# Kernel tuning notes

Measured on AMD Instinct MI355X. Metric: run time of the kernel, lower is better.

## Reference

```python
import jax, jax.numpy as jnp
import numpy as np

B, N = 8, 2048
DIN, DH, DE = 32, 64, 64
R = 3          # number_relations
L = 3          # num_layers -> 1 first + 1 block + 1 last
PRED_IN = DH * (L - 1) + DE  # concat: 64*2 + 64 = 192
EPS_BN = 1e-5
EPS_NORM = 1e-12


def setup_inputs() -> dict:
    key = jax.random.key(0)
    ks = jax.random.split(key, 12)
    x = jax.random.normal(ks[0], (B, N, DIN), jnp.float32)
    # relation labels in {0..R}; 0 = no edge, 1..R = relation type
    relation = jax.random.randint(ks[1], (B, N, N), 0, R + 1).astype(jnp.int32)
    # adjacency is the 0/1 edge indicator (float), as the torch code treats it
    adj = (relation > 0).astype(jnp.float32)
    s = 0.05
    w_first = jax.random.normal(ks[2], (R, DIN, DH), jnp.float32) * s
    b_first = jnp.zeros((DH,), jnp.float32)
    w_block = jax.random.normal(ks[3], (R, DH, DH), jnp.float32) * s
    b_block = jnp.zeros((DH,), jnp.float32)
    w_last = jax.random.normal(ks[4], (R, DH, DE), jnp.float32) * s
    b_last = jnp.zeros((DE,), jnp.float32)
    w_map = jax.random.normal(ks[5], (PRED_IN, DE), jnp.float32) * s
    b_map = jnp.zeros((DE,), jnp.float32)
    return {"x": x, "relation": relation, "adj": adj,
            "w_first": w_first, "b_first": b_first,
            "w_block": w_block, "b_block": b_block,
            "w_last": w_last, "b_last": b_last,
            "w_map": w_map, "b_map": b_map}


def _graph_conv(x, rel, W, b):
    # rel: [B,N,N] (int labels or float adjacency); W: [R, din, dout]
    y = jnp.zeros((x.shape[0], x.shape[1], W.shape[2]), x.dtype)
    for i in range(R):  # fixed, small relation count
        mask = (rel == (i + 1)).astype(x.dtype)            # [B,N,N]
        h = jnp.einsum('bij,bjd->bid', mask, x)            # masked aggregation
        y = y + jnp.einsum('bid,de->bie', h, W[i])
    y = y + b
    # F.normalize(p=2, dim=2): v / max(||v||, eps)
    nrm = jnp.sqrt(jnp.sum(y * y, axis=2, keepdims=True))
    return y / jnp.maximum(nrm, EPS_NORM)


def _apply_bn(x):
    # fresh BatchNorm1d(N) in training mode, affine weight=1/bias=0:
    # normalize over (batch, feature) per node index, biased variance
    mean = jnp.mean(x, axis=(0, 2), keepdims=True)
    var = jnp.mean(jnp.square(x - mean), axis=(0, 2), keepdims=True)
    return (x - mean) * jax.lax.rsqrt(var + EPS_BN)


def reference(x, relation, adj, w_first, b_first, w_block, b_block,
              w_last, b_last, w_map, b_map):
    # conv_first uses `relation`
    h = _apply_bn(jax.nn.relu(_graph_conv(x, relation, w_first, b_first)))
    out_all = [jnp.max(h, axis=1)]
    # conv_block and conv_last are (faithfully) called with `adj` as relation
    h = _apply_bn(jax.nn.relu(_graph_conv(h, adj, w_block, b_block)))
    out_all.append(jnp.max(h, axis=1))
    h = _graph_conv(h, adj, w_last, b_last)
    out_all.append(jnp.max(h, axis=1))
    output = jnp.concatenate(out_all, axis=1)        # [B, PRED_IN]
    ypred = output @ w_map + b_map                   # map_model Linear
    return (output, ypred)
```

## Files before the change

### kernel.cpp

```cpp
#include <hip/hip_runtime.h>


#define NN 2048
#define PLANE_W 1048576L

typedef short short8 __attribute__((ext_vector_type(8)));
typedef float floatx4 __attribute__((ext_vector_type(4)));

__device__ __forceinline__ unsigned short f2bf(float x) {
  unsigned u = __float_as_uint(x);
  u += 0x7FFFu + ((u >> 16) & 1u);
  return (unsigned short)(u >> 16);
}

__device__ void dev_xw_first(char* smemc, int u, int tid,
                             const float* __restrict__ x,
                             const float* __restrict__ w,
                             unsigned short* __restrict__ xws) {
  float* xs = (float*)smemc;
  float* wsh = (float*)(smemc + 64 * 33 * 4);
  const int jc = u & 31, b = (u >> 5) & 7, r = u >> 8;
  const int j0 = jc * 64;
  for (int idx = tid; idx < 64 * 32; idx += 256) {
    int row = idx >> 5, f = idx & 31;
    xs[row * 33 + f] = x[((long)b * NN + j0 + row) * 32 + f];
    wsh[idx] = w[r * 2048 + idx];
  }
  __syncthreads();
  const int j = tid & 63, g = tid >> 6;
  const int k = j0 + j;
  const int kblk = k >> 5, kq = (k >> 3) & 3, kj = k & 7;
  unsigned short* dst =
      xws + (((long)(r * 8 + b) * 64 + kblk) * 4 + g) * 512 + kj;
  float xr[32];
#pragma unroll
  for (int f = 0; f < 32; ++f) xr[f] = xs[j * 33 + f];
#pragma unroll
  for (int ii = 0; ii < 16; ++ii) {
    float acc = 0.f;
#pragma unroll
    for (int f = 0; f < 32; ++f) acc += xr[f] * wsh[f * 64 + g * 16 + ii];
    dst[(kq * 16 + ii) * 8] = f2bf(acc);
  }
  __syncthreads();
}

__global__ __launch_bounds__(256) void k_pack_xw1(const int* __restrict__ rel,
                                                  unsigned* __restrict__ planes,
                                                  const float* __restrict__ x,
                                                  const float* __restrict__ w,
                                                  unsigned short* __restrict__ xws) {
  __shared__ __align__(16) char smem[16640];
  const int bid = blockIdx.x, tid = threadIdx.x;
  if (bid < 768) dev_xw_first(smem, bid, tid, x, w, xws);
  for (long t = (long)bid * 256 + tid; t < 1048576L; t += 4096L * 256) {
    int w32 = (int)(t & 63);
    long bi = t >> 6;
    const int4* rp = (const int4*)(rel + bi * NN + w32 * 32);
    unsigned m0 = 0, m1 = 0, m2 = 0;
#pragma unroll
    for (int c = 0; c < 8; ++c) {
      int4 v = rp[c];
      int vv[4] = {v.x, v.y, v.z, v.w};
#pragma unroll
      for (int j = 0; j < 4; ++j) {
        unsigned b1 = 1u << (c * 4 + j);
        m0 |= (vv[j] == 1) ? b1 : 0u;
        m1 |= (vv[j] == 2) ? b1 : 0u;
        m2 |= (vv[j] == 3) ? b1 : 0u;
      }
    }
    long o = bi * 64 + w32;
    planes[o] = m0;
    planes[PLANE_W + o] = m1;
    planes[2 * PLANE_W + o] = m2;
  }
}

template <int NREL, bool RELU, bool POOL3>
__global__ __launch_bounds__(512) void k_gemm8(
    const unsigned* __restrict__ planes, const unsigned short* __restrict__ xws,
    const float* __restrict__ bias, float* __restrict__ Hout,
    float* __restrict__ part3) {
  constexpr int SMEM = (NREL * 8448 > 16640) ? NREL * 8448 : 16640;
  __shared__ __align__(16) char smem[SMEM];
  unsigned* mw = (unsigned*)smem;
  floatx4* cb = (floatx4*)smem;
  const int bid = blockIdx.x;
  const int b = bid & 7, it = bid >> 3;
  const int tid = threadIdx.x;
  const int wave = tid >> 6, lane = tid & 63;
  const int m = lane & 15, kq = lane >> 4;
  const int i0 = it * 64;

  floatx4 acc[4][4];
#pragma unroll
  for (int rs = 0; rs < 4; ++rs)
#pragma unroll
    for (int t = 0; t < 4; ++t) acc[rs][t] = floatx4{0, 0, 0, 0};

  for (int chunk = 0; chunk < 2; ++chunk) {
    for (int idx = tid; idx < NREL * 2048; idx += 512) {
      int p = idx >> 11, rem = idx & 2047, row = rem >> 5, w = rem & 31;
      long g = ((long)b * NN + i0 + row) * 64 + chunk * 32 + w;
      unsigned v;
      if (NREL == 3)
        v = planes[(long)p * PLANE_W + g];
      else
        v = planes[g] | planes[PLANE_W + g] | planes[2 * PLANE_W + g];
      mw[(p * 64 + row) * 33 + w] = v;
    }
    __syncthreads();
#pragma unroll
    for (int j = 0; j < 4; ++j) {
      const int kk = j * 8 + wave;
      const int kblk = chunk * 32 + kk;
#pragma unroll
      for (int p = 0; p < NREL; ++p) {
        const unsigned short* bb =
            xws + ((long)(p * 8 + b) * 64 + kblk) * 2048 + lane * 8;
        short8 bf0 = *(const short8*)(bb);
        short8 bf1 = *(const short8*)(bb + 512);
        short8 bf2 = *(const short8*)(bb + 1024);
        short8 bf3 = *(const short8*)(bb + 1536);
#pragma unroll
        for (int rs = 0; rs < 4; ++rs) {
          unsigned word = mw[(p * 64 + rs * 16 + m) * 33 + kk];
          unsigned byte = (word >> (kq * 8)) & 0xffu;
          unsigned pp = byte | (byte << 15);
          union {
            unsigned uu[4];
            short8 s8;
          } fr;
          unsigned w0 = pp & 0x00010001u;
          fr.uu[0] = (w0 << 14) - (w0 << 7);
          unsigned w1 = pp & 0x00040004u;
          fr.uu[1] = (w1 << 12) - (w1 << 5);
          unsigned w2 = pp & 0x00100010u;
          fr.uu[2] = (w2 << 10) - (w2 << 3);
          unsigned w3 = pp & 0x00400040u;
          fr.uu[3] = (w3 << 8) - (w3 << 1);
          acc[rs][0] = __builtin_amdgcn_mfma_f32_16x16x32_bf16(fr.s8, bf0,
                                                              acc[rs][0], 0, 0, 0);
          acc[rs][1] = __builtin_amdgcn_mfma_f32_16x16x32_bf16(fr.s8, bf1,
                                                              acc[rs][1], 0, 0, 0);
          acc[rs][2] = __builtin_amdgcn_mfma_f32_16x16x32_bf16(fr.s8, bf2,
                                                              acc[rs][2], 0, 0, 0);
          acc[rs][3] = __builtin_amdgcn_mfma_f32_16x16x32_bf16(fr.s8, bf3,
                                                              acc[rs][3], 0, 0, 0);
        }
      }
    }
    __syncthreads();
  }

  for (int k = 7; k >= 1; --k) {
    if (wave == k) {
      if (k == 7) {
#pragma unroll
        for (int rs = 0; rs < 4; ++rs)
#pragma unroll
          for (int t = 0; t < 4; ++t) cb[(rs * 4 + t) * 64 + lane] = acc[rs][t];
      } else {
#pragma unroll
        for (int rs = 0; rs < 4; ++rs)
#pragma unroll
          for (int t = 0; t < 4; ++t) {
            floatx4 v = cb[(rs * 4 + t) * 64 + lane];
            cb[(rs * 4 + t) * 64 + lane] = v + acc[rs][t];
          }
      }
    }
    __syncthreads();
  }
  if (wave == 0) {
#pragma unroll
    for (int rs = 0; rs < 4; ++rs)
#pragma unroll
      for (int t = 0; t < 4; ++t) acc[rs][t] += cb[(rs * 4 + t) * 64 + lane];
    float bv[4];
#pragma unroll
    for (int t = 0; t < 4; ++t) bv[t] = bias[t * 16 + m];
    float pmt[4] = {-3.4e38f, -3.4e38f, -3.4e38f, -3.4e38f};
#pragma unroll
    for (int rs = 0; rs < 4; ++rs) {
      float ss[4];
#pragma unroll
      for (int reg = 0; reg < 4; ++reg) {
#pragma unroll
        for (int t = 0; t < 4; ++t) acc[rs][t][reg] += bv[t];
        ss[reg] = acc[rs][0][reg] * acc[rs][0][reg] +
                  acc[rs][1][reg] * acc[rs][1][reg] +
                  acc[rs][2][reg] * acc[rs][2][reg] +
                  acc[rs][3][reg] * acc[rs][3][reg];
#pragma unroll
        for (int off = 1; off <= 8; off <<= 1)
          ss[reg] += __shfl_xor(ss[reg], off);
        ss[reg] = 1.0f / fmaxf(sqrtf(ss[reg]), 1e-12f);
      }
#pragma unroll
      for (int t = 0; t < 4; ++t) {
#pragma unroll
        for (int reg = 0; reg < 4; ++reg) {
          float o = acc[rs][t][reg] * ss[reg];
          if (RELU) o = fmaxf(o, 0.0f);
          if (POOL3)
            pmt[t] = fmaxf(pmt[t], o);
          else
            Hout[((long)b * NN + i0 + rs * 16 + kq * 4 + reg) * 64 + t * 16 + m] = o;
        }
      }
    }
    if (POOL3) {
#pragma unroll
      for (int t = 0; t < 4; ++t) {
        pmt[t] = fmaxf(pmt[t], __shfl_xor(pmt[t], 16));
        pmt[t] = fmaxf(pmt[t], __shfl_xor(pmt[t], 32));
      }
      if (kq == 0) {
#pragma unroll
        for (int t = 0; t < 4; ++t)
          part3[((long)b * 32 + it) * 64 + t * 16 + m] = pmt[t];
      }
    }
  }
}

__global__ __launch_bounds__(256) void k_xwh_bn(const float* __restrict__ H,
                                                const float* __restrict__ w,
                                                unsigned short* __restrict__ xws,
                                                float* __restrict__ PP) {
  __shared__ float hs[64 * 65];
  __shared__ float wsh[64 * 64];
  __shared__ float sm[64], srs[64];
  const int bid = blockIdx.x, tid = threadIdx.x;
  const int jc = bid & 31, b = bid >> 5;
  const int j0 = jc * 64;
  {
    const int n = tid >> 2, q = tid & 3;
    float s1 = 0.f, s2 = 0.f;
#pragma unroll
    for (int bb = 0; bb < 8; ++bb) {
      const float4* hp =
          (const float4*)(H + ((long)bb * NN + j0 + n) * 64 + q * 16);
#pragma unroll
      for (int c = 0; c < 4; ++c) {
        float4 v = hp[c];
        s1 += v.x + v.y + v.z + v.w;
        s2 += v.x * v.x + v.y * v.y + v.z * v.z + v.w * v.w;
      }
    }
    s1 += __shfl_xor(s1, 1);
    s2 += __shfl_xor(s2, 1);
    s1 += __shfl_xor(s1, 2);
    s2 += __shfl_xor(s2, 2);
    if (q == 0) {
      float mean = s1 * (1.0f / 512.0f);
      float var = fmaxf(s2 * (1.0f / 512.0f) - mean * mean, 0.0f);
      sm[n] = mean;
      srs[n] = rsqrtf(var + 1e-5f);
    }
  }
  __syncthreads();
  for (int idx = tid; idx < 4096; idx += 256) {
    int row = idx >> 6, f = idx & 63;
    float v = H[((long)b * NN + j0 + row) * 64 + f];
    hs[row * 65 + f] = (v - sm[row]) * srs[row];
    wsh[idx] = w[idx];
  }
  __syncthreads();
  {
    const int j = tid & 63, g = tid >> 6;
    const int k = j0 + j;
    const int kblk = k >> 5, kq = (k >> 3) & 3, kj = k & 7;
    unsigned short* dst = xws + (((long)b * 64 + kblk) * 4 + g) * 512 + kj;
    float acc[16];
#pragma unroll
    for (int ii = 0; ii < 16; ++ii) acc[ii] = 0.f;
#pragma unroll
    for (int c = 0; c < 4; ++c) {
      float xr[16];
#pragma unroll
      for (int f = 0; f < 16; ++f) xr[f] = hs[j * 65 + c * 16 + f];
#pragma unroll
      for (int ii = 0; ii < 16; ++ii)
#pragma unroll
        for (int f = 0; f < 16; ++f)
          acc[ii] += xr[f] * wsh[(c * 16 + f) * 64 + g * 16 + ii];
    }
#pragma unroll
    for (int ii = 0; ii < 16; ++ii) dst[(kq * 16 + ii) * 8] = f2bf(acc[ii]);
  }
  if (b == 0) {
#pragma unroll
    for (int part = 0; part < 2; ++part) {
      const int col = part * 256 + tid;
      const int bb = col >> 6, e = col & 63;
      float mx = -3.4e38f;
      for (int n = 0; n < 64; ++n) {
        float v = H[((long)bb * NN + j0 + n) * 64 + e];
        mx = fmaxf(mx, (v - sm[n]) * srs[n]);
      }
      PP[(long)jc * 512 + col] = mx;
    }
  }
}

__global__ __launch_bounds__(512) void k_tail(const float* __restrict__ PP1,
                                              const float* __restrict__ PP2,
                                              const float* __restrict__ P3,
                                              float* __restrict__ out,
                                              const float* __restrict__ wmap,
                                              const float* __restrict__ bmap) {
  const int col = threadIdx.x;
  const int bb = col >> 6, e = col & 63;
  float m1 = -3.4e38f, m2 = -3.4e38f, m3 = -3.4e38f;
#pragma unroll
  for (int c = 0; c < 32; ++c) {
    m1 = fmaxf(m1, PP1[(long)c * 512 + col]);
    m2 = fmaxf(m2, PP2[(long)c * 512 + col]);
    m3 = fmaxf(m3, P3[((long)bb * 32 + c) * 64 + e]);
  }
  out[bb * 192 + e] = m1;
  out[bb * 192 + 64 + e] = m2;
  out[bb * 192 + 128 + e] = m3;
  __syncthreads();
  float acc = bmap[e];
  for (int k = 0; k < 192; ++k) acc += out[bb * 192 + k] * wmap[k * 64 + e];
  out[1536 + bb * 64 + e] = acc;
}

extern "C" void kernel_launch(void* const* d_in, const int* in_sizes, int n_in,
                              void* d_out, int out_size, void* d_ws,
                              size_t ws_size, hipStream_t stream) {
  const float* x = (const float*)d_in[0];
  const int* rel = (const int*)d_in[1];
  const float* w_first = (const float*)d_in[3];
  const float* b_first = (const float*)d_in[4];
  const float* w_block = (const float*)d_in[5];
  const float* b_block = (const float*)d_in[6];
  const float* w_last = (const float*)d_in[7];
  const float* b_last = (const float*)d_in[8];
  const float* w_map = (const float*)d_in[9];
  const float* b_map = (const float*)d_in[10];
  float* out = (float*)d_out;

  char* ws = (char*)d_ws;
  const size_t MB = 1024 * 1024;
  unsigned* PLANES = (unsigned*)(ws);
  unsigned short* XWS = (unsigned short*)(ws + 12 * MB);
  float* H = (float*)(ws + 18 * MB);
  float* PP1 = (float*)(ws + 22 * MB);
  float* PP2 = (float*)(ws + 23 * MB);
  float* PART3 = (float*)(ws + 24 * MB);

  k_pack_xw1<<<4096, 256, 0, stream>>>(rel, PLANES, x, w_first, XWS);
  k_gemm8<3, true, false><<<256, 512, 0, stream>>>(PLANES, XWS, b_first, H,
                                                   nullptr);
  k_xwh_bn<<<256, 256, 0, stream>>>(H, w_block, XWS, PP1);
  k_gemm8<1, true, false><<<256, 512, 0, stream>>>(PLANES, XWS, b_block, H,
                                                   nullptr);
  k_xwh_bn<<<256, 256, 0, stream>>>(H, w_last, XWS, PP2);
  k_gemm8<1, false, true><<<256, 512, 0, stream>>>(PLANES, XWS, b_last,
                                                   nullptr, PART3);
  k_tail<<<1, 512, 0, stream>>>(PP1, PP2, PART3, out, w_map, b_map);
}
```

Baseline: 353.3 us.

## Fuse all layers into one persistent kernel with dataflow counter synchronization

Replaces the seven-launch pipeline with a single persistent kernel of 256 blocks that packs relation bitplanes directly into shared memory, keeps them resident across all three graph-conv layers, and coordinates phases with per-batch and per-tile atomic counters instead of kernel boundaries. The packed relation planes are no longer written to and re-read from global memory, and launch gaps between stages are removed. In exchange, the kernel relies on all 256 blocks being co-resident for the spin-waits to progress, and it adds a 64KB shared allocation and fences.

```diff
diff --git a/kernel.cpp b/kernel.cpp
--- a/kernel.cpp
+++ b/kernel.cpp
@@ -2,7 +2,6 @@
 
 
 #define NN 2048
-#define PLANE_W 1048576L
 
 typedef short short8 __attribute__((ext_vector_type(8)));
 typedef float floatx4 __attribute__((ext_vector_type(4)));
@@ -13,81 +12,32 @@
   return (unsigned short)(u >> 16);
 }
 
-__device__ void dev_xw_first(char* smemc, int u, int tid,
-                             const float* __restrict__ x,
-                             const float* __restrict__ w,
-                             unsigned short* __restrict__ xws) {
-  float* xs = (float*)smemc;
-  float* wsh = (float*)(smemc + 64 * 33 * 4);
-  const int jc = u & 31, b = (u >> 5) & 7, r = u >> 8;
-  const int j0 = jc * 64;
-  for (int idx = tid; idx < 64 * 32; idx += 256) {
-    int row = idx >> 5, f = idx & 31;
-    xs[row * 33 + f] = x[((long)b * NN + j0 + row) * 32 + f];
-    wsh[idx] = w[r * 2048 + idx];
-  }
-  __syncthreads();
-  const int j = tid & 63, g = tid >> 6;
-  const int k = j0 + j;
-  const int kblk = k >> 5, kq = (k >> 3) & 3, kj = k & 7;
-  unsigned short* dst =
-      xws + (((long)(r * 8 + b) * 64 + kblk) * 4 + g) * 512 + kj;
-  float xr[32];
-#pragma unroll
-  for (int f = 0; f < 32; ++f) xr[f] = xs[j * 33 + f];
-#pragma unroll
-  for (int ii = 0; ii < 16; ++ii) {
-    float acc = 0.f;
-#pragma unroll
-    for (int f = 0; f < 32; ++f) acc += xr[f] * wsh[f * 64 + g * 16 + ii];
-    dst[(kq * 16 + ii) * 8] = f2bf(acc);
-  }
-  __syncthreads();
-}
-
-__global__ __launch_bounds__(256) void k_pack_xw1(const int* __restrict__ rel,
-                                                  unsigned* __restrict__ planes,
-                                                  const float* __restrict__ x,
-                                                  const float* __restrict__ w,
-                                                  unsigned short* __restrict__ xws) {
-  __shared__ __align__(16) char smem[16640];
-  const int bid = blockIdx.x, tid = threadIdx.x;
-  if (bid < 768) dev_xw_first(smem, bid, tid, x, w, xws);
-  for (long t = (long)bid * 256 + tid; t < 1048576L; t += 4096L * 256) {
-    int w32 = (int)(t & 63);
-    long bi = t >> 6;
-    const int4* rp = (const int4*)(rel + bi * NN + w32 * 32);
-    unsigned m0 = 0, m1 = 0, m2 = 0;
-#pragma unroll
-    for (int c = 0; c < 8; ++c) {
-      int4 v = rp[c];
-      int vv[4] = {v.x, v.y, v.z, v.w};
-#pragma unroll
-      for (int j = 0; j < 4; ++j) {
-        unsigned b1 = 1u << (c * 4 + j);
-        m0 |= (vv[j] == 1) ? b1 : 0u;
-        m1 |= (vv[j] == 2) ? b1 : 0u;
-        m2 |= (vv[j] == 3) ? b1 : 0u;
-      }
-    }
-    long o = bi * 64 + w32;
-    planes[o] = m0;
-    planes[PLANE_W + o] = m1;
-    planes[2 * PLANE_W + o] = m2;
-  }
+__device__ __forceinline__ float bf2f(unsigned short v) {
+  return __uint_as_float(((unsigned)v) << 16);
+}
+
+__device__ __forceinline__ void bump(unsigned* c) {
+  __threadfence();
+  __syncthreads();
+  if (threadIdx.x == 0)
+    __hip_atomic_fetch_add(c, 1u, __ATOMIC_RELEASE, __HIP_MEMORY_SCOPE_AGENT);
+}
+
+__device__ __forceinline__ void waitc(unsigned* c, unsigned tgt) {
+  if (threadIdx.x == 0) {
+    while (__hip_atomic_load(c, __ATOMIC_RELAXED, __HIP_MEMORY_SCOPE_AGENT) < tgt)
+      __builtin_amdgcn_s_sleep(1);
+  }
+  __syncthreads();
+  __threadfence();
 }
 
 template <int NREL, bool RELU, bool POOL3>
-__global__ __launch_bounds__(512) void k_gemm8(
-    const unsigned* __restrict__ planes, const unsigned short* __restrict__ xws,
-    const float* __restrict__ bias, float* __restrict__ Hout,
-    float* __restrict__ part3) {
-  constexpr int SMEM = (NREL * 8448 > 16640) ? NREL * 8448 : 16640;
-  __shared__ __align__(16) char smem[SMEM];
-  unsigned* mw = (unsigned*)smem;
-  floatx4* cb = (floatx4*)smem;
-  const int bid = blockIdx.x;
-  const int b = bid & 7, it = bid >> 3;
+__device__ void gemm_phase(const unsigned* __restrict__ mloc, char* scratch,
+                           const unsigned short* __restrict__ xwsL,
+                           const float* __restrict__ bias,
+                           float* __restrict__ Hout, float* __restrict__ part3,
+                           int b, int it) {
   const int tid = threadIdx.x;
   const int wave = tid >> 6, lane = tid & 63;
   const int m = lane & 15, kq = lane >> 4;
@@ -99,61 +49,47 @@
 #pragma unroll
     for (int t = 0; t < 4; ++t) acc[rs][t] = floatx4{0, 0, 0, 0};
 
-  for (int chunk = 0; chunk < 2; ++chunk) {
-    for (int idx = tid; idx < NREL * 2048; idx += 512) {
-      int p = idx >> 11, rem = idx & 2047, row = rem >> 5, w = rem & 31;
-      long g = ((long)b * NN + i0 + row) * 64 + chunk * 32 + w;
-      unsigned v;
-      if (NREL == 3)
-        v = planes[(long)p * PLANE_W + g];
-      else
-        v = planes[g] | planes[PLANE_W + g] | planes[2 * PLANE_W + g];
-      mw[(p * 64 + row) * 33 + w] = v;
-    }
-    __syncthreads();
-#pragma unroll
-    for (int j = 0; j < 4; ++j) {
-      const int kk = j * 8 + wave;
-      const int kblk = chunk * 32 + kk;
-#pragma unroll
-      for (int p = 0; p < NREL; ++p) {
-        const unsigned short* bb =
-            xws + ((long)(p * 8 + b) * 64 + kblk) * 2048 + lane * 8;
-        short8 bf0 = *(const short8*)(bb);
-        short8 bf1 = *(const short8*)(bb + 512);
-        short8 bf2 = *(const short8*)(bb + 1024);
-        short8 bf3 = *(const short8*)(bb + 1536);
-#pragma unroll
-        for (int rs = 0; rs < 4; ++rs) {
-          unsigned word = mw[(p * 64 + rs * 16 + m) * 33 + kk];
-          unsigned byte = (word >> (kq * 8)) & 0xffu;
-          unsigned pp = byte | (byte << 15);
-          union {
-            unsigned uu[4];
-            short8 s8;
-          } fr;
-          unsigned w0 = pp & 0x00010001u;
-          fr.uu[0] = (w0 << 14) - (w0 << 7);
-          unsigned w1 = pp & 0x00040004u;
-          fr.uu[1] = (w1 << 12) - (w1 << 5);
-          unsigned w2 = pp & 0x00100010u;
-          fr.uu[2] = (w2 << 10) - (w2 << 3);
-          unsigned w3 = pp & 0x00400040u;
-          fr.uu[3] = (w3 << 8) - (w3 << 1);
-          acc[rs][0] = __builtin_amdgcn_mfma_f32_16x16x32_bf16(fr.s8, bf0,
-                                                              acc[rs][0], 0, 0, 0);
-          acc[rs][1] = __builtin_amdgcn_mfma_f32_16x16x32_bf16(fr.s8, bf1,
-                                                              acc[rs][1], 0, 0, 0);
-          acc[rs][2] = __builtin_amdgcn_mfma_f32_16x16x32_bf16(fr.s8, bf2,
-                                                              acc[rs][2], 0, 0, 0);
-          acc[rs][3] = __builtin_amdgcn_mfma_f32_16x16x32_bf16(fr.s8, bf3,
-                                                              acc[rs][3], 0, 0, 0);
-        }
-      }
-    }
-    __syncthreads();
-  }
-
+  for (int kk8 = 0; kk8 < 8; ++kk8) {
+    const int kblk = kk8 * 8 + wave;
+#pragma unroll
+    for (int p = 0; p < NREL; ++p) {
+      const unsigned short* bb2 =
+          xwsL + ((long)(p * 8 + b) * 64 + kblk) * 2048 + lane * 8;
+      short8 bf0 = *(const short8*)(bb2);
+      short8 bf1 = *(const short8*)(bb2 + 512);
+      short8 bf2 = *(const short8*)(bb2 + 1024);
+      short8 bf3 = *(const short8*)(bb2 + 1536);
+#pragma unroll
+      for (int rs = 0; rs < 4; ++rs) {
+        const int row = rs * 16 + m;
+        unsigned word = mloc[p * 4096 + row * 64 + (kblk ^ (row & 31))];
+        unsigned byte = (word >> (kq * 8)) & 0xffu;
+        unsigned pp = byte | (byte << 15);
+        union {
+          unsigned uu[4];
+          short8 s8;
+        } fr;
+        unsigned w0 = pp & 0x00010001u;
+        fr.uu[0] = (w0 << 14) - (w0 << 7);
+        unsigned w1 = pp & 0x00040004u;
+        fr.uu[1] = (w1 << 12) - (w1 << 5);
+        unsigned w2 = pp & 0x00100010u;
+        fr.uu[2] = (w2 << 10) - (w2 << 3);
+        unsigned w3 = pp & 0x00400040u;
+        fr.uu[3] = (w3 << 8) - (w3 << 1);
+        acc[rs][0] = __builtin_amdgcn_mfma_f32_16x16x32_bf16(fr.s8, bf0,
+                                                             acc[rs][0], 0, 0, 0);
+        acc[rs][1] = __builtin_amdgcn_mfma_f32_16x16x32_bf16(fr.s8, bf1,
+                                                             acc[rs][1], 0, 0, 0);
+        acc[rs][2] = __builtin_amdgcn_mfma_f32_16x16x32_bf16(fr.s8, bf2,
+                                                             acc[rs][2], 0, 0, 0);
+        acc[rs][3] = __builtin_amdgcn_mfma_f32_16x16x32_bf16(fr.s8, bf3,
+                                                             acc[rs][3], 0, 0, 0);
+      }
+    }
+  }
+  __syncthreads();
+  floatx4* cb = (floatx4*)scratch;
   for (int k = 7; k >= 1; --k) {
     if (wave == k) {
       if (k == 7) {
@@ -226,108 +162,189 @@
   }
 }
 
-__global__ __launch_bounds__(256) void k_xwh_bn(const float* __restrict__ H,
-                                                const float* __restrict__ w,
-                                                unsigned short* __restrict__ xws,
-                                                float* __restrict__ PP) {
-  __shared__ float hs[64 * 65];
-  __shared__ float wsh[64 * 64];
-  __shared__ float sm[64], srs[64];
-  const int bid = blockIdx.x, tid = threadIdx.x;
-  const int jc = bid & 31, b = bid >> 5;
-  const int j0 = jc * 64;
+__device__ void bnxw_phase(char* scratch, const float* __restrict__ Hsrc,
+                           const float* __restrict__ wmat,
+                           unsigned short* __restrict__ xwsD,
+                           float* __restrict__ PPdst, int b, int it) {
+  float* hs = (float*)scratch;
+  float* wsh = (float*)(scratch + 16640);
+  float* smean = (float*)(scratch + 33024);
+  float* srsv = (float*)(scratch + 33280);
+  const int tid = threadIdx.x;
+  const int i0 = it * 64;
   {
-    const int n = tid >> 2, q = tid & 3;
+    const int n = tid >> 3, s = tid & 7;
+    const float4* hp = (const float4*)(Hsrc + ((long)s * NN + i0 + n) * 64);
     float s1 = 0.f, s2 = 0.f;
 #pragma unroll
-    for (int bb = 0; bb < 8; ++bb) {
-      const float4* hp =
-          (const float4*)(H + ((long)bb * NN + j0 + n) * 64 + q * 16);
-#pragma unroll
-      for (int c = 0; c < 4; ++c) {
-        float4 v = hp[c];
-        s1 += v.x + v.y + v.z + v.w;
-        s2 += v.x * v.x + v.y * v.y + v.z * v.z + v.w * v.w;
-      }
-    }
-    s1 += __shfl_xor(s1, 1);
-    s2 += __shfl_xor(s2, 1);
-    s1 += __shfl_xor(s1, 2);
-    s2 += __shfl_xor(s2, 2);
-    if (q == 0) {
+    for (int c = 0; c < 16; ++c) {
+      float4 v = hp[c];
+      s1 += v.x + v.y + v.z + v.w;
+      s2 += v.x * v.x + v.y * v.y + v.z * v.z + v.w * v.w;
+    }
+    s1 += __shfl_xor(s1, 1); s2 += __shfl_xor(s2, 1);
+    s1 += __shfl_xor(s1, 2); s2 += __shfl_xor(s2, 2);
+    s1 += __shfl_xor(s1, 4); s2 += __shfl_xor(s2, 4);
+    if (s == 0) {
       float mean = s1 * (1.0f / 512.0f);
       float var = fmaxf(s2 * (1.0f / 512.0f) - mean * mean, 0.0f);
-      sm[n] = mean;
-      srs[n] = rsqrtf(var + 1e-5f);
-    }
-  }
-  __syncthreads();
-  for (int idx = tid; idx < 4096; idx += 256) {
+      smean[n] = mean;
+      srsv[n] = rsqrtf(var + 1e-5f);
+    }
+  }
+  __syncthreads();
+  for (int idx = tid; idx < 4096; idx += 512) {
     int row = idx >> 6, f = idx & 63;
-    float v = H[((long)b * NN + j0 + row) * 64 + f];
-    hs[row * 65 + f] = (v - sm[row]) * srs[row];
-    wsh[idx] = w[idx];
+    float v = Hsrc[((long)b * NN + i0 + row) * 64 + f];
+    hs[row * 65 + f] = (v - smean[row]) * srsv[row];
+    wsh[idx] = wmat[idx];
   }
   __syncthreads();
   {
-    const int j = tid & 63, g = tid >> 6;
-    const int k = j0 + j;
-    const int kblk = k >> 5, kq = (k >> 3) & 3, kj = k & 7;
-    unsigned short* dst = xws + (((long)b * 64 + kblk) * 4 + g) * 512 + kj;
-    float acc[16];
-#pragma unroll
-    for (int ii = 0; ii < 16; ++ii) acc[ii] = 0.f;
-#pragma unroll
-    for (int c = 0; c < 4; ++c) {
-      float xr[16];
-#pragma unroll
-      for (int f = 0; f < 16; ++f) xr[f] = hs[j * 65 + c * 16 + f];
-#pragma unroll
-      for (int ii = 0; ii < 16; ++ii)
-#pragma unroll
-        for (int f = 0; f < 16; ++f)
-          acc[ii] += xr[f] * wsh[(c * 16 + f) * 64 + g * 16 + ii];
-    }
-#pragma unroll
-    for (int ii = 0; ii < 16; ++ii) dst[(kq * 16 + ii) * 8] = f2bf(acc[ii]);
+    const int j = tid & 63, gg = tid >> 6;
+    const int k = i0 + j;
+    const int kblk = k >> 5, kqq = (k >> 3) & 3, kj = k & 7;
+    float xr[64];
+#pragma unroll
+    for (int f = 0; f < 64; ++f) xr[f] = hs[j * 65 + f];
+#pragma unroll
+    for (int ii = 0; ii < 8; ++ii) {
+      const int e = gg * 8 + ii;
+      float a = 0.f;
+#pragma unroll
+      for (int f = 0; f < 64; ++f) a += xr[f] * wsh[f * 64 + e];
+      xwsD[(((long)b * 64 + kblk) * 4 + (e >> 4)) * 512 +
+           (kqq * 16 + (e & 15)) * 8 + kj] = f2bf(a);
+    }
   }
   if (b == 0) {
-#pragma unroll
-    for (int part = 0; part < 2; ++part) {
-      const int col = part * 256 + tid;
-      const int bb = col >> 6, e = col & 63;
-      float mx = -3.4e38f;
-      for (int n = 0; n < 64; ++n) {
-        float v = H[((long)bb * NN + j0 + n) * 64 + e];
-        mx = fmaxf(mx, (v - sm[n]) * srs[n]);
-      }
-      PP[(long)jc * 512 + col] = mx;
-    }
-  }
-}
-
-__global__ __launch_bounds__(512) void k_tail(const float* __restrict__ PP1,
-                                              const float* __restrict__ PP2,
-                                              const float* __restrict__ P3,
-                                              float* __restrict__ out,
-                                              const float* __restrict__ wmap,
-                                              const float* __restrict__ bmap) {
-  const int col = threadIdx.x;
-  const int bb = col >> 6, e = col & 63;
-  float m1 = -3.4e38f, m2 = -3.4e38f, m3 = -3.4e38f;
-#pragma unroll
-  for (int c = 0; c < 32; ++c) {
-    m1 = fmaxf(m1, PP1[(long)c * 512 + col]);
-    m2 = fmaxf(m2, PP2[(long)c * 512 + col]);
-    m3 = fmaxf(m3, P3[((long)bb * 32 + c) * 64 + e]);
-  }
-  out[bb * 192 + e] = m1;
-  out[bb * 192 + 64 + e] = m2;
-  out[bb * 192 + 128 + e] = m3;
-  __syncthreads();
-  float acc = bmap[e];
-  for (int k = 0; k < 192; ++k) acc += out[bb * 192 + k] * wmap[k * 64 + e];
-  out[1536 + bb * 64 + e] = acc;
+    const int bb = tid >> 6, e = tid & 63;
+    float mx = -3.4e38f;
+    for (int n = 0; n < 64; ++n) {
+      float v = Hsrc[((long)bb * NN + i0 + n) * 64 + e];
+      mx = fmaxf(mx, (v - smean[n]) * srsv[n]);
+    }
+    PPdst[(long)it * 512 + tid] = mx;
+  }
+}
+
+__global__ __launch_bounds__(512, 2) void gcn_df(
+    const float* __restrict__ x, const int* __restrict__ rel,
+    const float* __restrict__ w_first, const float* __restrict__ b_first,
+    const float* __restrict__ w_block, const float* __restrict__ b_block,
+    const float* __restrict__ w_last, const float* __restrict__ b_last,
+    const float* __restrict__ w_map, const float* __restrict__ b_map,
+    float* __restrict__ out, unsigned short* __restrict__ XWS1,
+    unsigned short* __restrict__ XWS2, unsigned short* __restrict__ XWS3,
+    float* __restrict__ H1, float* __restrict__ H2, float* __restrict__ PP1,
+    float* __restrict__ PP2, float* __restrict__ PART3,
+    unsigned* __restrict__ cnt) {
+  __shared__ __align__(16) char smem[65536];
+  unsigned* uplane = (unsigned*)smem;
+  char* scratch = smem + 16384;
+  const int bid = blockIdx.x, tid = threadIdx.x;
+  const int b = bid & 7, it = bid >> 3;
+  const int i0 = it * 64;
+
+  {
+    float* xs = (float*)scratch;
+    float* wsh = (float*)(scratch + 8448);
+    for (int idx = tid; idx < 2048; idx += 512) {
+      int row = idx >> 5, f = idx & 31;
+      xs[row * 33 + f] = x[((long)b * NN + i0 + row) * 32 + f];
+    }
+    __syncthreads();
+    const int j = tid & 63, gg = tid >> 6;
+    const int k = i0 + j;
+    const int kblk = k >> 5, kqq = (k >> 3) & 3, kj = k & 7;
+    float xr[32];
+#pragma unroll
+    for (int f = 0; f < 32; ++f) xr[f] = xs[j * 33 + f];
+    for (int r = 0; r < 3; ++r) {
+      for (int idx = tid; idx < 2048; idx += 512) wsh[idx] = w_first[r * 2048 + idx];
+      __syncthreads();
+#pragma unroll
+      for (int ii = 0; ii < 8; ++ii) {
+        const int e = gg * 8 + ii;
+        float a = 0.f;
+#pragma unroll
+        for (int f = 0; f < 32; ++f) a += xr[f] * wsh[f * 64 + e];
+        XWS1[(((long)(r * 8 + b) * 64 + kblk) * 4 + (e >> 4)) * 512 +
+             (kqq * 16 + (e & 15)) * 8 + kj] = f2bf(a);
+      }
+      __syncthreads();
+    }
+  }
+  {
+    unsigned* mw3 = (unsigned*)scratch;
+    const int row = tid >> 3, seg = tid & 7;
+    const int rsw = row & 31;
+    const long base = ((long)b * NN + i0 + row) * NN + seg * 256;
+#pragma unroll
+    for (int w8 = 0; w8 < 8; ++w8) {
+      const int w = seg * 8 + w8;
+      const int4* rp = (const int4*)(rel + base + w8 * 32);
+      unsigned m0 = 0, m1 = 0, m2 = 0;
+#pragma unroll
+      for (int c = 0; c < 8; ++c) {
+        int4 v = rp[c];
+        int vv[4] = {v.x, v.y, v.z, v.w};
+#pragma unroll
+        for (int q = 0; q < 4; ++q) {
+          unsigned bit = 1u << (c * 4 + q);
+          m0 |= (vv[q] == 1) ? bit : 0u;
+          m1 |= (vv[q] == 2) ? bit : 0u;
+          m2 |= (vv[q] == 3) ? bit : 0u;
+        }
+      }
+      const int off = row * 64 + (w ^ rsw);
+      mw3[off] = m0;
+      mw3[4096 + off] = m1;
+      mw3[8192 + off] = m2;
+      uplane[off] = m0 | m1 | m2;
+    }
+  }
+  bump(&cnt[b]);
+
+  waitc(&cnt[b], 32);
+  gemm_phase<3, true, false>((unsigned*)scratch, scratch, XWS1, b_first, H1,
+                             nullptr, b, it);
+  bump(&cnt[8 + it]);
+
+  waitc(&cnt[8 + it], 8);
+  bnxw_phase(scratch, H1, w_block, XWS2, PP1, b, it);
+  bump(&cnt[40 + b]);
+
+  waitc(&cnt[40 + b], 32);
+  gemm_phase<1, true, false>(uplane, scratch, XWS2, b_block, H2, nullptr, b, it);
+  bump(&cnt[48 + it]);
+
+  waitc(&cnt[48 + it], 8);
+  bnxw_phase(scratch, H2, w_last, XWS3, PP2, b, it);
+  bump(&cnt[80 + b]);
+
+  waitc(&cnt[80 + b], 32);
+  gemm_phase<1, false, true>(uplane, scratch, XWS3, b_last, nullptr, PART3, b, it);
+  bump(&cnt[88]);
+
+  if (bid == 0) {
+    waitc(&cnt[88], 256);
+    const int bb = tid >> 6, e = tid & 63;
+    float m1 = -3.4e38f, m2 = -3.4e38f, m3 = -3.4e38f;
+#pragma unroll
+    for (int c = 0; c < 32; ++c) {
+      m1 = fmaxf(m1, PP1[(long)c * 512 + tid]);
+      m2 = fmaxf(m2, PP2[(long)c * 512 + tid]);
+      m3 = fmaxf(m3, PART3[((long)bb * 32 + c) * 64 + e]);
+    }
+    out[bb * 192 + e] = m1;
+    out[bb * 192 + 64 + e] = m2;
+    out[bb * 192 + 128 + e] = m3;
+    __syncthreads();
+    float a = b_map[e];
+    for (int k = 0; k < 192; ++k) a += out[bb * 192 + k] * w_map[k * 64 + e];
+    out[1536 + bb * 64 + e] = a;
+  }
 }
 
 extern "C" void kernel_launch(void* const* d_in, const int* in_sizes, int n_in,
@@ -347,21 +364,18 @@
 
   char* ws = (char*)d_ws;
   const size_t MB = 1024 * 1024;
-  unsigned* PLANES = (unsigned*)(ws);
-  unsigned short* XWS = (unsigned short*)(ws + 12 * MB);
-  float* H = (float*)(ws + 18 * MB);
-  float* PP1 = (float*)(ws + 22 * MB);
-  float* PP2 = (float*)(ws + 23 * MB);
-  float* PART3 = (float*)(ws + 24 * MB);
-
-  k_pack_xw1<<<4096, 256, 0, stream>>>(rel, PLANES, x, w_first, XWS);
-  k_gemm8<3, true, false><<<256, 512, 0, stream>>>(PLANES, XWS, b_first, H,
-                                                   nullptr);
-  k_xwh_bn<<<256, 256, 0, stream>>>(H, w_block, XWS, PP1);
-  k_gemm8<1, true, false><<<256, 512, 0, stream>>>(PLANES, XWS, b_block, H,
-                                                   nullptr);
-  k_xwh_bn<<<256, 256, 0, stream>>>(H, w_last, XWS, PP2);
-  k_gemm8<1, false, true><<<256, 512, 0, stream>>>(PLANES, XWS, b_last,
-                                                   nullptr, PART3);
-  k_tail<<<1, 512, 0, stream>>>(PP1, PP2, PART3, out, w_map, b_map);
-}
+  unsigned short* XWS1 = (unsigned short*)(ws);
+  unsigned short* XWS2 = (unsigned short*)(ws + 6 * MB);
+  unsigned short* XWS3 = (unsigned short*)(ws + 8 * MB);
+  float* H1 = (float*)(ws + 10 * MB);
+  float* H2 = (float*)(ws + 14 * MB);
+  float* PP1 = (float*)(ws + 18 * MB);
+  float* PP2 = (float*)(ws + 19 * MB);
+  float* PART3 = (float*)(ws + 20 * MB);
+  unsigned* CNT = (unsigned*)(ws + 21 * MB);
+
+  hipMemsetAsync((void*)CNT, 0, 512, stream);
+  gcn_df<<<256, 512, 0, stream>>>(x, rel, w_first, b_first, w_block, b_block,
+                                  w_last, b_last, w_map, b_map, out, XWS1,
+                                  XWS2, XWS3, H1, H2, PP1, PP2, PART3, CNT);
+}
```

After: 807.0 us. +128.4%, slower.
